# Optimization experiments

Hardware: AMD Instinct MI355X
Metric: run time of the kernel (lower is better)

Reference implementation:

```python
import jax, jax.numpy as jnp
import numpy as np

N = 50000
E = 800000
DIN = 256
DH = 256
DOUT = 256
R = 8
B = 4


def setup_inputs() -> dict:
    key = jax.random.key(0)
    ks = jax.random.split(key, 12)
    s = 0.05
    return {
        "x": jax.random.normal(ks[0], (N, DIN), jnp.float32),
        "edge_index": jax.random.randint(ks[1], (2, E), 0, N, jnp.int64),
        "edge_type": jax.random.randint(ks[2], (E,), 0, R, jnp.int64),
        "basis1": jax.random.normal(ks[3], (B, DIN, DH), jnp.float32) * s,
        "comp1": jax.random.normal(ks[4], (R, B), jnp.float32) * s,
        "root1": jax.random.normal(ks[5], (DIN, DH), jnp.float32) * s,
        "bias1": jnp.zeros((DH,), jnp.float32),
        "basis2": jax.random.normal(ks[6], (B, DH, DOUT), jnp.float32) * s,
        "comp2": jax.random.normal(ks[7], (R, B), jnp.float32) * s,
        "root2": jax.random.normal(ks[8], (DH, DOUT), jnp.float32) * s,
        "bias2": jnp.zeros((DOUT,), jnp.float32),
    }


def rgcn_conv(x, src, dst, edge_type, basis, comp, root, bias):
    # Basis-decomposed relational conv (PyG RGCNConv, aggr='mean').
    # xb: per-node transform by each basis matrix -> [N, B, out]
    xb = jnp.einsum('ni,bio->nbo', x, basis)
    # Per-edge message: mix bases with relation coefficients -> [E, out]
    msg = jnp.einsum('eb,ebo->eo', comp[edge_type], xb[src])
    # Mean aggregation per (dst, relation): divide each edge by the count of
    # edges of its relation arriving at its destination, then scatter-add.
    key = dst * R + edge_type
    cnt = jax.ops.segment_sum(jnp.ones((msg.shape[0],), x.dtype), key,
                              num_segments=x.shape[0] * R)
    norm = 1.0 / jnp.maximum(cnt, 1.0)
    agg = jax.ops.segment_sum(msg * norm[key][:, None], dst,
                              num_segments=x.shape[0])
    return agg + x @ root + bias


def reference(x, edge_index, edge_type, basis1, comp1, root1, bias1,
              basis2, comp2, root2, bias2):
    src, dst = edge_index[0], edge_index[1]
    h = rgcn_conv(x, src, dst, edge_type, basis1, comp1, root1, bias1)
    h = jax.nn.relu(h)
    # dropout(p=0.4) is identity in eval mode
    out = rgcn_conv(h, src, dst, edge_type, basis2, comp2, root2, bias2)
    return out
```

## Files before the change

### kernel.cpp

```cpp
#include <hip/hip_runtime.h>
#include <hip/hip_bf16.h>

constexpr int N_NODES = 50000;
constexpr int N_EDGES = 800000;
constexpr int R_REL   = 8;
constexpr int BASES   = 4;
constexpr int D       = 256;
constexpr int KZ      = BASES * D;
constexpr int KT      = KZ + D;
constexpr int WSTRIDE = 16;
constexpr int DUMMY_P = 8 << 20;

constexpr int BUCK   = 128;
constexpr int NHI    = (N_NODES + BUCK - 1) / BUCK;
constexpr int NS_BLK = 400;
constexpr int CH     = N_EDGES / NS_BLK;

constexpr int CB4 = (N_NODES * 128) / 1024;
constexpr int WKB = KT / 64;
constexpr int CAP = N_EDGES + N_NODES * 8;
constexpr int FB4 = (CAP + 1023) / 1024;

typedef __attribute__((ext_vector_type(8))) short bf16x8;
typedef __attribute__((ext_vector_type(4))) float f32x4;

__device__ inline float bfu_lo(unsigned u) { return __uint_as_float(u << 16); }
__device__ inline float bfu_hi(unsigned u) { return __uint_as_float(u & 0xFFFF0000u); }
__device__ inline unsigned short f2bu(float f) {
  __hip_bfloat16 h = __float2bfloat16(f);
  return *reinterpret_cast<unsigned short*>(&h);
}
__device__ inline void store_out(float* p, float v) { *p = v; }
__device__ inline void store_out(__hip_bfloat16* p, float v) { *p = __float2bfloat16(v); }

__device__ inline void gload_lds16(void* lds, const void* g) {
  __builtin_amdgcn_global_load_lds(
      (const __attribute__((address_space(1))) unsigned*)g,
      (__attribute__((address_space(3))) unsigned*)lds, 16, 0, 0);
}

__device__ inline void scan512(int* sd, int tid) {
  for (int off = 1; off < 512; off <<= 1) {
    int a = (tid >= off) ? sd[tid - off] : 0;
    int b = (tid + 256 >= off) ? sd[tid + 256 - off] : 0;
    __syncthreads();
    sd[tid] += a;
    sd[tid + 256] += b;
    __syncthreads();
  }
}

__global__ __launch_bounds__(256) void prep_kernel(
    const int* __restrict__ ei,
    int* __restrict__ ghist,
    const float* __restrict__ x, unsigned* __restrict__ x2,
    const float* __restrict__ basis1, const float* __restrict__ root1,
    __hip_bfloat16* __restrict__ WT1,
    const float* __restrict__ basis2, const float* __restrict__ root2,
    __hip_bfloat16* __restrict__ WT2,
    int* __restrict__ packed) {
  __shared__ __hip_bfloat16 tile[16][256];
  __shared__ int hist[NHI];
  int bid = blockIdx.x;
  int tid = threadIdx.x;

  if (bid < NS_BLK) {
    for (int k = tid; k < NHI; k += 256) hist[k] = 0;
    __syncthreads();
    int start = bid * CH;
    for (int i = start + tid; i < start + CH; i += 256)
      atomicAdd(&hist[ei[N_EDGES + i] >> 7], 1);
    __syncthreads();
    for (int k = tid; k < NHI; k += 256)
      ghist[(size_t)k * NS_BLK + bid] = hist[k];
    return;
  }
  bid -= NS_BLK;
  if (bid < CB4) {
    int idx = (bid * 256 + tid) * 4;
    const float* px = x + (size_t)idx * 2;
    float4 a = *(const float4*)(px);
    float4 b = *(const float4*)(px + 4);
    uint4 o;
    o.x = (unsigned)f2bu(a.x) | ((unsigned)f2bu(a.y) << 16);
    o.y = (unsigned)f2bu(a.z) | ((unsigned)f2bu(a.w) << 16);
    o.z = (unsigned)f2bu(b.x) | ((unsigned)f2bu(b.y) << 16);
    o.w = (unsigned)f2bu(b.z) | ((unsigned)f2bu(b.w) << 16);
    *(uint4*)(x2 + idx) = o;
    return;
  }
  bid -= CB4;
  if (bid < 2 * WKB) {
    const float* basis = (bid < WKB) ? basis1 : basis2;
    const float* root  = (bid < WKB) ? root1 : root2;
    __hip_bfloat16* WT = (bid < WKB) ? WT1 : WT2;
    int wb = (bid < WKB) ? bid : bid - WKB;
    int k0 = wb * 64;
#pragma unroll
    for (int pass = 0; pass < 4; pass++) {
      int kp = k0 + pass * 16;
#pragma unroll
      for (int r = 0; r < 16; r++) {
        int k = kp + r;
        const float* srow = (k < KZ)
            ? basis + ((size_t)(k & 3) * D + (k >> 2)) * D
            : root + (size_t)(k - KZ) * D;
        tile[r][tid] = __float2bfloat16(srow[tid]);
      }
      __syncthreads();
      __hip_bfloat16* dst = WT + (size_t)tid * KT + kp;
#pragma unroll
      for (int c = 0; c < 2; c++) {
        union { short s[8]; int4 v; } u;
#pragma unroll
        for (int r = 0; r < 8; r++)
          u.s[r] = *reinterpret_cast<short*>(&tile[c * 8 + r][tid]);
        *(int4*)(dst + c * 8) = u.v;
      }
      __syncthreads();
    }
    return;
  }
  bid -= 2 * WKB;
  {
    int i = (bid * 256 + tid) * 4;
    if (i < CAP) {
      int4 f = make_int4(DUMMY_P, DUMMY_P, DUMMY_P, DUMMY_P);
      *(int4*)(packed + i) = f;
    }
  }
}

__global__ __launch_bounds__(256) void binprefix_kernel(
    const int* __restrict__ ghist, int* __restrict__ boffs,
    int* __restrict__ bintot) {
  __shared__ int sd[512];
  int b = blockIdx.x;
  int tid = threadIdx.x;
  int v0 = (tid < NS_BLK) ? ghist[(size_t)b * NS_BLK + tid] : 0;
  int v1 = (tid + 256 < NS_BLK) ? ghist[(size_t)b * NS_BLK + tid + 256] : 0;
  sd[tid] = v0;
  sd[tid + 256] = v1;
  __syncthreads();
  scan512(sd, tid);
  if (tid < NS_BLK) boffs[(size_t)b * NS_BLK + tid] = sd[tid] - v0;
  if (tid + 256 < NS_BLK)
    boffs[(size_t)b * NS_BLK + tid + 256] = sd[tid + 256] - v1;
  if (tid == 255) bintot[b] = sd[511];
}

__global__ __launch_bounds__(256) void coarse_scatter_kernel(
    const int* __restrict__ ei, const int* __restrict__ et,
    const int* __restrict__ bintot, const int* __restrict__ boffs,
    int* __restrict__ coarse) {
  __shared__ int lbase[NHI];
  __shared__ int lcnt[NHI];
  __shared__ int sd[512];
  int bid = blockIdx.x;
  int tid = threadIdx.x;
  for (int k = tid; k < NHI; k += 256) lcnt[k] = 0;
  int v0 = (tid < NHI) ? bintot[tid] : 0;
  int v1 = (tid + 256 < NHI) ? bintot[tid + 256] : 0;
  sd[tid] = v0;
  sd[tid + 256] = v1;
  __syncthreads();
  scan512(sd, tid);
  if (tid < NHI) lbase[tid] = (sd[tid] - v0) + boffs[(size_t)tid * NS_BLK + bid];
  if (tid + 256 < NHI)
    lbase[tid + 256] =
        (sd[tid + 256] - v1) + boffs[(size_t)(tid + 256) * NS_BLK + bid];
  __syncthreads();
  int start = bid * CH;
  for (int i = start + tid; i < start + CH; i += 256) {
    int src = ei[i];
    int dst = ei[N_EDGES + i];
    int rt  = et[i];
    int bin = dst >> 7;
    int rank = atomicAdd(&lcnt[bin], 1);
    coarse[lbase[bin] + rank] = src | (rt << 16) | ((dst & 127) << 19);
  }
}

__global__ __launch_bounds__(256) void fine_hist_kernel(
    const int* __restrict__ coarse, const int* __restrict__ bintot,
    const float* __restrict__ comp1, float4* __restrict__ wtab1,
    const float* __restrict__ comp2, float4* __restrict__ wtab2,
    int* __restrict__ lestart, int* __restrict__ btot) {
  __shared__ int c2[BUCK * R_REL];
  __shared__ int sd[512];
  int b = blockIdx.x;
  int tid = threadIdx.x;
#pragma unroll
  for (int k = tid; k < BUCK * R_REL; k += 256) c2[k] = 0;
  int v0 = (tid < NHI) ? bintot[tid] : 0;
  int v1 = (tid + 256 < NHI) ? bintot[tid + 256] : 0;
  sd[tid] = v0;
  sd[tid + 256] = v1;
  __syncthreads();
  scan512(sd, tid);
  int n_e = bintot[b];
  int cbase = sd[b] - n_e;
  __syncthreads();
  for (int i = tid; i < n_e; i += 256) {
    int e = coarse[cbase + i];
    int key = ((e >> 19) & 127) * R_REL + ((e >> 16) & 7);
    atomicAdd(&c2[key], 1);
  }
  __syncthreads();
  int nodebase = b * BUCK;
  for (int k = tid; k < BUCK * WSTRIDE; k += 256) {
    int lo = k >> 4, r = k & (WSTRIDE - 1);
    int n = nodebase + lo;
    if (n < N_NODES) {
      float4 w1 = make_float4(0.f, 0.f, 0.f, 0.f);
      float4 w2 = w1;
      if (r < R_REL) {
        int c = c2[lo * R_REL + r];
        float inv = 1.0f / (float)(c > 0 ? c : 1);
        w1.x = comp1[r * BASES + 0] * inv;
        w1.y = comp1[r * BASES + 1] * inv;
        w1.z = comp1[r * BASES + 2] * inv;
        w1.w = comp1[r * BASES + 3] * inv;
        w2.x = comp2[r * BASES + 0] * inv;
        w2.y = comp2[r * BASES + 1] * inv;
        w2.z = comp2[r * BASES + 2] * inv;
        w2.w = comp2[r * BASES + 3] * inv;
      }
      wtab1[(size_t)n * WSTRIDE + r] = w1;
      wtab2[(size_t)n * WSTRIDE + r] = w2;
    }
  }
  int d = 0;
  if (tid < BUCK) {
#pragma unroll
    for (int r = 0; r < R_REL; r++) d += c2[tid * R_REL + r];
  }
  int dp = (d + 7) & ~7;
  __syncthreads();
  sd[tid] = dp;
  __syncthreads();
  for (int off = 1; off < 256; off <<= 1) {
    int t = (tid >= off) ? sd[tid - off] : 0;
    __syncthreads();
    sd[tid] += t;
    __syncthreads();
  }
  if (tid < BUCK) lestart[b * BUCK + tid] = sd[tid] - dp;
  if (tid == 255) btot[b] = sd[255];
}

__global__ __launch_bounds__(256) void fine_scatter_kernel(
    const int* __restrict__ coarse, const int* __restrict__ bintot,
    const int* __restrict__ btot, const int* __restrict__ lestart,
    int* __restrict__ estart, int* __restrict__ packed) {
  __shared__ int lest[BUCK];
  __shared__ int lcur[BUCK];
  __shared__ int sd[512];
  int b = blockIdx.x;
  int tid = threadIdx.x;
  if (tid < BUCK) {
    lest[tid] = lestart[b * BUCK + tid];
    lcur[tid] = 0;
  }
  int v0 = (tid < NHI) ? bintot[tid] : 0;
  int v1 = (tid + 256 < NHI) ? bintot[tid + 256] : 0;
  sd[tid] = v0;
  sd[tid + 256] = v1;
  __syncthreads();
  scan512(sd, tid);
  int n_e = bintot[b];
  int cbase = sd[b] - n_e;
  __syncthreads();
  int w0 = (tid < NHI) ? btot[tid] : 0;
  int w1 = (tid + 256 < NHI) ? btot[tid + 256] : 0;
  sd[tid] = w0;
  sd[tid + 256] = w1;
  __syncthreads();
  scan512(sd, tid);
  int bt = btot[b];
  int bb = sd[b] - bt;
  __syncthreads();
  {
    int n = b * BUCK + tid;
    if (tid < BUCK && n < N_NODES) estart[n] = bb + lest[tid];
    if (b == NHI - 1 && tid == 0) estart[N_NODES] = bb + bt;
  }
  __syncthreads();
  for (int i = tid; i < n_e; i += 256) {
    int e = coarse[cbase + i];
    int lo = (e >> 19) & 127;
    int rank = atomicAdd(&lcur[lo], 1);
    packed[bb + lest[lo] + rank] = (e & 0xFFFF) | (((e >> 16) & 7) << 20);
  }
}

__device__ inline float2 pfma(float s, float2 a, float2 c) {
  c.x = fmaf(s, a.x, c.x);
  c.y = fmaf(s, a.y, c.y);
  return c;
}

__device__ inline void edge_fma(float2 acc[BASES][2], uint2 v, float4 w) {
  float2 a01 = make_float2(bfu_lo(v.x), bfu_hi(v.x));
  float2 a23 = make_float2(bfu_lo(v.y), bfu_hi(v.y));
  acc[0][0] = pfma(w.x, a01, acc[0][0]); acc[0][1] = pfma(w.x, a23, acc[0][1]);
  acc[1][0] = pfma(w.y, a01, acc[1][0]); acc[1][1] = pfma(w.y, a23, acc[1][1]);
  acc[2][0] = pfma(w.z, a01, acc[2][0]); acc[2][1] = pfma(w.z, a23, acc[2][1]);
  acc[3][0] = pfma(w.w, a01, acc[3][0]); acc[3][1] = pfma(w.w, a23, acc[3][1]);
}

__global__ __launch_bounds__(256) void aggregate_kernel(
    const unsigned* __restrict__ x2,
    const int* __restrict__ packed,
    const int* __restrict__ estart,
    const float4* __restrict__ wtab,
    __hip_bfloat16* __restrict__ zA,
    int n0)
{
  int tid = threadIdx.x;
  int lane = tid & 63;
  int n = __builtin_amdgcn_readfirstlane(n0 + blockIdx.x * 4 + (tid >> 6));
  int s = __builtin_amdgcn_readfirstlane(estart[n]);
  int e = __builtin_amdgcn_readfirstlane(estart[n + 1]);
  const int voff = lane * 2;
  const float4* wt = wtab + (size_t)n * WSTRIDE;

  float2 acc[BASES][2] = {};

  for (int base = s; base < e; base += 8) {
    int4 q0 = *(const int4*)(packed + base);
    int4 q1 = *(const int4*)(packed + base + 4);
    int p0 = __builtin_amdgcn_readfirstlane(q0.x);
    int p1 = __builtin_amdgcn_readfirstlane(q0.y);
    int p2 = __builtin_amdgcn_readfirstlane(q0.z);
    int p3 = __builtin_amdgcn_readfirstlane(q0.w);
    int p4 = __builtin_amdgcn_readfirstlane(q1.x);
    int p5 = __builtin_amdgcn_readfirstlane(q1.y);
    int p6 = __builtin_amdgcn_readfirstlane(q1.z);
    int p7 = __builtin_amdgcn_readfirstlane(q1.w);
    const unsigned* r0 = x2 + ((size_t)(p0 & 0xFFFFF) << 7);
    const unsigned* r1 = x2 + ((size_t)(p1 & 0xFFFFF) << 7);
    const unsigned* r2 = x2 + ((size_t)(p2 & 0xFFFFF) << 7);
    const unsigned* r3 = x2 + ((size_t)(p3 & 0xFFFFF) << 7);
    const unsigned* r4 = x2 + ((size_t)(p4 & 0xFFFFF) << 7);
    const unsigned* r5 = x2 + ((size_t)(p5 & 0xFFFFF) << 7);
    const unsigned* r6 = x2 + ((size_t)(p6 & 0xFFFFF) << 7);
    const unsigned* r7 = x2 + ((size_t)(p7 & 0xFFFFF) << 7);
    uint2 v0 = *(const uint2*)(r0 + voff);
    uint2 v1 = *(const uint2*)(r1 + voff);
    uint2 v2 = *(const uint2*)(r2 + voff);
    uint2 v3 = *(const uint2*)(r3 + voff);
    uint2 v4 = *(const uint2*)(r4 + voff);
    uint2 v5 = *(const uint2*)(r5 + voff);
    uint2 v6 = *(const uint2*)(r6 + voff);
    uint2 v7 = *(const uint2*)(r7 + voff);
    float4 w0 = wt[p0 >> 20];
    float4 w1 = wt[p1 >> 20];
    float4 w2 = wt[p2 >> 20];
    float4 w3 = wt[p3 >> 20];
    float4 w4 = wt[p4 >> 20];
    float4 w5 = wt[p5 >> 20];
    float4 w6 = wt[p6 >> 20];
    float4 w7 = wt[p7 >> 20];
    edge_fma(acc, v0, w0);
    edge_fma(acc, v1, w1);
    edge_fma(acc, v2, w2);
    edge_fma(acc, v3, w3);
    edge_fma(acc, v4, w4);
    edge_fma(acc, v5, w5);
    edge_fma(acc, v6, w6);
    edge_fma(acc, v7, w7);
  }

  union { short s[8]; int4 v; } u0, u1;
#pragma unroll
  for (int b = 0; b < BASES; b++) {
    u0.s[b]     = (short)f2bu(acc[b][0].x);
    u0.s[4 + b] = (short)f2bu(acc[b][0].y);
    u1.s[b]     = (short)f2bu(acc[b][1].x);
    u1.s[4 + b] = (short)f2bu(acc[b][1].y);
  }
  __hip_bfloat16* zrow = zA + (size_t)n * KZ;
  *(int4*)(zrow + 16 * lane) = u0.v;
  *(int4*)(zrow + 16 * lane + 8) = u1.v;
}

#define BM 128
#define BN 256
#define BK 32

template <bool RELU, typename OutT>
__global__ __launch_bounds__(512) void gemm_kernel(
    const __hip_bfloat16* __restrict__ Az,
    const __hip_bfloat16* __restrict__ Aself,
    const __hip_bfloat16* __restrict__ Bt,
    const float* __restrict__ bias, OutT* __restrict__ C, int M) {
  __shared__ __align__(16) __hip_bfloat16 As[2][BM * BK];
  __shared__ __align__(16) __hip_bfloat16 Bs[2][BN * BK];
  int tid = threadIdx.x;
  int m0 = blockIdx.x * BM;
  int wave = tid >> 6, lane = tid & 63;
  int wm = wave & 1, wn = wave >> 1;
  int l15 = lane & 15, quad = lane >> 4;

  int colS = (lane & 3) * 8;
  int rowA = wave * 16 + (lane >> 2);
  int grA  = min(m0 + rowA, M - 1);
  const __hip_bfloat16* gAz = Az + (size_t)grA * KZ + colS;
  const __hip_bfloat16* gAs = Aself + (size_t)grA * D + colS;
  const __hip_bfloat16* gB0 = Bt + (size_t)(wave * 32 + (lane >> 2)) * KT + colS;
  const __hip_bfloat16* gB1 = gB0 + 16 * KT;

  f32x4 acc[4][4] = {};

  auto stage = [&](int buf, int k0) {
    const __hip_bfloat16* srcA = (k0 < KZ) ? (gAz + k0) : (gAs + (k0 - KZ));
    gload_lds16(As[buf] + wave * 512, srcA);
    gload_lds16(Bs[buf] + wave * 1024, gB0 + k0);
    gload_lds16(Bs[buf] + wave * 1024 + 512, gB1 + k0);
  };

  stage(0, 0);
  int cur = 0;
  for (int k0 = 0; k0 < KT; k0 += BK) {
    if (k0 + BK < KT) {
      stage(cur ^ 1, k0 + BK);
      asm volatile("s_waitcnt vmcnt(3)" ::: "memory");
    } else {
      asm volatile("s_waitcnt vmcnt(0)" ::: "memory");
    }
    __builtin_amdgcn_s_barrier();
    __builtin_amdgcn_sched_barrier(0);

    bf16x8 af[4], bfr[4];
#pragma unroll
    for (int mt = 0; mt < 4; mt++)
      af[mt] = *(const bf16x8*)(As[cur] + (wm * 64 + mt * 16 + l15) * BK + quad * 8);
#pragma unroll
    for (int nt = 0; nt < 4; nt++)
      bfr[nt] = *(const bf16x8*)(Bs[cur] + (wn * 64 + nt * 16 + l15) * BK + quad * 8);
#pragma unroll
    for (int mt = 0; mt < 4; mt++)
#pragma unroll
      for (int nt = 0; nt < 4; nt++)
        acc[mt][nt] = __builtin_amdgcn_mfma_f32_16x16x32_bf16(
            af[mt], bfr[nt], acc[mt][nt], 0, 0, 0);
    __builtin_amdgcn_s_barrier();
    cur ^= 1;
  }

#pragma unroll
  for (int nt = 0; nt < 4; nt++) {
    int cg = wn * 64 + nt * 16 + l15;
    float bv = bias[cg];
#pragma unroll
    for (int mt = 0; mt < 4; mt++) {
#pragma unroll
      for (int r = 0; r < 4; r++) {
        int rg = m0 + wm * 64 + mt * 16 + quad * 4 + r;
        if (rg < M) {
          float v = acc[mt][nt][r] + bv;
          if (RELU) v = fmaxf(v, 0.f);
          store_out(C + (size_t)rg * D + cg, v);
        }
      }
    }
  }
}

static inline char* carve(char*& p, size_t bytes) {
  char* r = p;
  p += (bytes + 255) & ~(size_t)255;
  return r;
}

extern "C" void kernel_launch(void* const* d_in, const int* in_sizes, int n_in,
                              void* d_out, int out_size, void* d_ws,
                              size_t ws_size, hipStream_t stream) {
  const float* x      = (const float*)d_in[0];
  const int*   ei     = (const int*)d_in[1];
  const int*   et     = (const int*)d_in[2];
  const float* basis1 = (const float*)d_in[3];
  const float* comp1  = (const float*)d_in[4];
  const float* root1  = (const float*)d_in[5];
  const float* bias1  = (const float*)d_in[6];
  const float* basis2 = (const float*)d_in[7];
  const float* comp2  = (const float*)d_in[8];
  const float* root2  = (const float*)d_in[9];
  const float* bias2  = (const float*)d_in[10];
  float* out = (float*)d_out;

  char* ws = (char*)d_ws;
  int* estart  = (int*)carve(ws, (size_t)(N_NODES + 1) * 4);
  int* coarse  = (int*)carve(ws, (size_t)N_EDGES * 4);
  int* ghist   = (int*)carve(ws, (size_t)NHI * NS_BLK * 4);
  int* boffs   = (int*)carve(ws, (size_t)NHI * NS_BLK * 4);
  int* bintot  = (int*)carve(ws, 512 * 4);
  int* btot    = (int*)carve(ws, 512 * 4);
  int* lestart = (int*)carve(ws, (size_t)NHI * BUCK * 4);
  int* packed  = (int*)carve(ws, (size_t)CAP * 4);
  float4* wtab1 = (float4*)carve(ws, (size_t)N_NODES * WSTRIDE * 16);
  float4* wtab2 = (float4*)carve(ws, (size_t)N_NODES * WSTRIDE * 16);
  __hip_bfloat16* WT1 = (__hip_bfloat16*)carve(ws, (size_t)D * KT * 2);
  __hip_bfloat16* WT2 = (__hip_bfloat16*)carve(ws, (size_t)D * KT * 2);
  unsigned* xb = (unsigned*)carve(ws, (size_t)N_NODES * D * 2);
  __hip_bfloat16* h = (__hip_bfloat16*)carve(ws, (size_t)N_NODES * D * 2);
  __hip_bfloat16* zA = (__hip_bfloat16*)carve(ws, (size_t)N_NODES * KZ * 2);

  prep_kernel<<<NS_BLK + CB4 + 2 * WKB + FB4, 256, 0, stream>>>(
      ei, ghist, x, xb, basis1, root1, WT1, basis2, root2, WT2, packed);
  binprefix_kernel<<<NHI, 256, 0, stream>>>(ghist, boffs, bintot);
  coarse_scatter_kernel<<<NS_BLK, 256, 0, stream>>>(ei, et, bintot, boffs,
                                                    coarse);
  fine_hist_kernel<<<NHI, 256, 0, stream>>>(coarse, bintot, comp1, wtab1,
                                            comp2, wtab2, lestart, btot);
  fine_scatter_kernel<<<NHI, 256, 0, stream>>>(coarse, bintot, btot, lestart,
                                               estart, packed);

  dim3 ggrid((N_NODES + BM - 1) / BM, 1);
  const int HALF = N_NODES / 2;
  const int AH = HALF / 4;

  aggregate_kernel<<<AH, 256, 0, stream>>>(xb, packed, estart, wtab1, zA, 0);
  aggregate_kernel<<<AH, 256, 0, stream>>>(xb, packed, estart, wtab1, zA, HALF);
  gemm_kernel<true, __hip_bfloat16><<<ggrid, 512, 0, stream>>>(
      zA, (const __hip_bfloat16*)xb, WT1, bias1, h, N_NODES);

  aggregate_kernel<<<AH, 256, 0, stream>>>((const unsigned*)h, packed, estart,
                                           wtab2, zA, 0);
  aggregate_kernel<<<AH, 256, 0, stream>>>((const unsigned*)h, packed, estart,
                                           wtab2, zA, HALF);
  gemm_kernel<false, float><<<ggrid, 512, 0, stream>>>(
      zA, h, WT2, bias2, out, N_NODES);
}
```

Measured before the change: 439.7 us.

## Split GEMM tile across N halves and swizzle LDS reads against bank conflicts

The fused GEMM now uses 256-thread blocks that each compute a 128x128 output tile, with two blocks per row tile covering the two column halves. This doubles the grid and should improve occupancy and load balance across CUs. LDS layout also gets an XOR swizzle on the 16-byte chunk slot, applied both when staging global loads and when reading fragments, to reduce bank conflicts. In exchange, the A operand is now loaded twice, once per column-half block, which adds global and L2 traffic.

```diff
diff --git a/kernel.cpp b/kernel.cpp
--- a/kernel.cpp
+++ b/kernel.cpp
@@ -386,46 +386,56 @@
 }
 
 #define BM 128
-#define BN 256
+#define BNH 128
 #define BK 32
 
 template <bool RELU, typename OutT>
-__global__ __launch_bounds__(512) void gemm_kernel(
+__global__ __launch_bounds__(256) void gemm_kernel(
     const __hip_bfloat16* __restrict__ Az,
     const __hip_bfloat16* __restrict__ Aself,
     const __hip_bfloat16* __restrict__ Bt,
     const float* __restrict__ bias, OutT* __restrict__ C, int M) {
   __shared__ __align__(16) __hip_bfloat16 As[2][BM * BK];
-  __shared__ __align__(16) __hip_bfloat16 Bs[2][BN * BK];
-  int tid = threadIdx.x;
-  int m0 = blockIdx.x * BM;
+  __shared__ __align__(16) __hip_bfloat16 Bs[2][BNH * BK];
+  int tid = threadIdx.x;
+  int m0 = (blockIdx.x >> 1) * BM;
+  int n0 = (blockIdx.x & 1) * BNH;
   int wave = tid >> 6, lane = tid & 63;
   int wm = wave & 1, wn = wave >> 1;
   int l15 = lane & 15, quad = lane >> 4;
 
-  int colS = (lane & 3) * 8;
-  int rowA = wave * 16 + (lane >> 2);
-  int grA  = min(m0 + rowA, M - 1);
-  const __hip_bfloat16* gAz = Az + (size_t)grA * KZ + colS;
-  const __hip_bfloat16* gAs = Aself + (size_t)grA * D + colS;
-  const __hip_bfloat16* gB0 = Bt + (size_t)(wave * 32 + (lane >> 2)) * KT + colS;
-  const __hip_bfloat16* gB1 = gB0 + 16 * KT;
+  int srcslot = ((lane & 3) ^ ((lane >> 3) & 3)) * 8;
+  int rA0 = wave * 32 + (lane >> 2);
+  int rA1 = rA0 + 16;
+  int gr0 = min(m0 + rA0, M - 1);
+  int gr1 = min(m0 + rA1, M - 1);
+  const __hip_bfloat16* gAz0 = Az + (size_t)gr0 * KZ + srcslot;
+  const __hip_bfloat16* gAz1 = Az + (size_t)gr1 * KZ + srcslot;
+  const __hip_bfloat16* gAs0 = Aself + (size_t)gr0 * D + srcslot;
+  const __hip_bfloat16* gAs1 = Aself + (size_t)gr1 * D + srcslot;
+  const __hip_bfloat16* gB0 = Bt + (size_t)(n0 + rA0) * KT + srcslot;
+  const __hip_bfloat16* gB1 = Bt + (size_t)(n0 + rA1) * KT + srcslot;
 
   f32x4 acc[4][4] = {};
 
   auto stage = [&](int buf, int k0) {
-    const __hip_bfloat16* srcA = (k0 < KZ) ? (gAz + k0) : (gAs + (k0 - KZ));
-    gload_lds16(As[buf] + wave * 512, srcA);
+    const __hip_bfloat16 *a0, *a1;
+    if (k0 < KZ) { a0 = gAz0 + k0; a1 = gAz1 + k0; }
+    else         { a0 = gAs0 + (k0 - KZ); a1 = gAs1 + (k0 - KZ); }
+    gload_lds16(As[buf] + wave * 1024, a0);
+    gload_lds16(As[buf] + wave * 1024 + 512, a1);
     gload_lds16(Bs[buf] + wave * 1024, gB0 + k0);
     gload_lds16(Bs[buf] + wave * 1024 + 512, gB1 + k0);
   };
+
+  int rswz = (quad ^ ((l15 >> 1) & 3)) * 8;
 
   stage(0, 0);
   int cur = 0;
   for (int k0 = 0; k0 < KT; k0 += BK) {
     if (k0 + BK < KT) {
       stage(cur ^ 1, k0 + BK);
-      asm volatile("s_waitcnt vmcnt(3)" ::: "memory");
+      asm volatile("s_waitcnt vmcnt(4)" ::: "memory");
     } else {
       asm volatile("s_waitcnt vmcnt(0)" ::: "memory");
     }
@@ -435,10 +445,10 @@
     bf16x8 af[4], bfr[4];
 #pragma unroll
     for (int mt = 0; mt < 4; mt++)
-      af[mt] = *(const bf16x8*)(As[cur] + (wm * 64 + mt * 16 + l15) * BK + quad * 8);
+      af[mt] = *(const bf16x8*)(As[cur] + (wm * 64 + mt * 16 + l15) * BK + rswz);
 #pragma unroll
     for (int nt = 0; nt < 4; nt++)
-      bfr[nt] = *(const bf16x8*)(Bs[cur] + (wn * 64 + nt * 16 + l15) * BK + quad * 8);
+      bfr[nt] = *(const bf16x8*)(Bs[cur] + (wn * 64 + nt * 16 + l15) * BK + rswz);
 #pragma unroll
     for (int mt = 0; mt < 4; mt++)
 #pragma unroll
@@ -451,7 +461,7 @@
 
 #pragma unroll
   for (int nt = 0; nt < 4; nt++) {
-    int cg = wn * 64 + nt * 16 + l15;
+    int cg = n0 + wn * 64 + nt * 16 + l15;
     float bv = bias[cg];
 #pragma unroll
     for (int mt = 0; mt < 4; mt++) {
@@ -517,19 +527,19 @@
   fine_scatter_kernel<<<NHI, 256, 0, stream>>>(coarse, bintot, btot, lestart,
                                                estart, packed);
 
-  dim3 ggrid((N_NODES + BM - 1) / BM, 1);
+  dim3 ggrid(((N_NODES + BM - 1) / BM) * 2, 1);
   const int HALF = N_NODES / 2;
   const int AH = HALF / 4;
 
   aggregate_kernel<<<AH, 256, 0, stream>>>(xb, packed, estart, wtab1, zA, 0);
   aggregate_kernel<<<AH, 256, 0, stream>>>(xb, packed, estart, wtab1, zA, HALF);
-  gemm_kernel<true, __hip_bfloat16><<<ggrid, 512, 0, stream>>>(
+  gemm_kernel<true, __hip_bfloat16><<<ggrid, 256, 0, stream>>>(
       zA, (const __hip_bfloat16*)xb, WT1, bias1, h, N_NODES);
 
   aggregate_kernel<<<AH, 256, 0, stream>>>((const unsigned*)h, packed, estart,
                                            wtab2, zA, 0);
   aggregate_kernel<<<AH, 256, 0, stream>>>((const unsigned*)h, packed, estart,
                                            wtab2, zA, HALF);
-  gemm_kernel<false, float><<<ggrid, 512, 0, stream>>>(
+  gemm_kernel<false, float><<<ggrid, 256, 0, stream>>>(
       zA, h, WT2, bias2, out, N_NODES);
 }
```

Result: slower. 498.3 us (+13.3%).
